# Optimization experiments

Measured on AMD Instinct MI355X. Metric: run time of the kernel, lower is better.

The kernel has to match this reference:

```python
import jax, jax.numpy as jnp
import numpy as np

N, E, H, FN, FE, FO, L = 20000, 50000, 32, 4, 2, 4, 3

def _gelu(v):
    return jax.nn.gelu(v, approximate=False)  # torch nn.GELU default = exact erf

def setup_inputs() -> dict:
    key = jax.random.key(0)
    ks = jax.random.split(key, 24)
    def w(k, shape, fan_in):
        return jax.random.normal(k, shape, dtype=jnp.float32) / np.sqrt(fan_in)
    inp = {
        "x": jax.random.normal(ks[0], (N, FN), dtype=jnp.float32),
        "pred_mask": (jax.random.uniform(ks[1], (N, FN)) < 0.5).astype(jnp.float32),
        "edge_index": jax.random.randint(ks[2], (2, E), 0, N, dtype=jnp.int64),
        "edge_attr": jax.random.normal(ks[3], (E, FE), dtype=jnp.float32),
        # input encoder
        "W_in": w(ks[4], (FN, H), FN), "b_in": jnp.zeros((H,), jnp.float32),
        # mask embedding MLP
        "mW1": w(ks[5], (FN, H), FN), "mb1": jnp.zeros((H,), jnp.float32),
        "mW2": w(ks[6], (H, H), H),   "mb2": jnp.zeros((H,), jnp.float32),
        # per-layer stacked params (leading dim L)
        "eW1": w(ks[7], (L, FE, H), FE),    "eb1": jnp.zeros((L, H), jnp.float32),
        "eW2": w(ks[8], (L, H, H * H), H),  "eb2": jnp.zeros((L, H * H), jnp.float32),
        "W_root": w(ks[9], (L, H, H), H),   "conv_b": jnp.zeros((L, H), jnp.float32),
        "gamma": jnp.ones((L, H), jnp.float32), "beta": jnp.zeros((L, H), jnp.float32),
        # output decoder
        "dW1": w(ks[10], (H, H), H),  "db1": jnp.zeros((H,), jnp.float32),
        "dW2": w(ks[11], (H, FO), H), "db2": jnp.zeros((FO,), jnp.float32),
    }
    return inp

def reference(x, pred_mask, edge_index, edge_attr,
              W_in, b_in, mW1, mb1, mW2, mb2,
              eW1, eb1, eW2, eb2, W_root, conv_b, gamma, beta,
              dW1, db1, dW2, db2):
    # input projection + mask embedding
    h = x @ W_in + b_in + (_gelu(pred_mask @ mW1 + mb1) @ mW2 + mb2)
    # undirect graph (random edge list is directed -> torch path duplicates)
    src = jnp.concatenate([edge_index[0], edge_index[1]])  # [2E]
    dst = jnp.concatenate([edge_index[1], edge_index[0]])
    ea = jnp.concatenate([edge_attr, edge_attr], axis=0)    # [2E, FE]

    def layer(h, p):
        w1, b1, w2, b2, wr, cb, g, b = p
        # edge-conditioned weights: [2E, H, H]
        ew = (_gelu(ea @ w1 + b1) @ w2 + b2).reshape(-1, H, H)
        msg = jnp.einsum('eh,eho->eo', h[src], ew)          # gather + per-edge matvec
        agg = jax.ops.segment_sum(msg, dst, num_segments=N) # scatter-add
        hc = agg + h @ wr + cb                               # NNConv root weight + bias
        mu = jnp.mean(hc, axis=-1, keepdims=True)
        var = jnp.var(hc, axis=-1, keepdims=True)
        hn = (hc - mu) * jax.lax.rsqrt(var + 1e-5) * g + b   # LayerNorm
        return h + _gelu(hn), None                           # dropout in eval mode (no-op)

    h, _ = jax.lax.scan(layer, h, (eW1, eb1, eW2, eb2, W_root, conv_b, gamma, beta))
    out = _gelu(h @ dW1 + db1) @ dW2 + db2
    return out
```

## Files before the change

### kernel.cpp

```cpp
#include <hip/hip_runtime.h>
#include <hip/hip_bf16.h>
#include <math.h>

#define NN  20000
#define NE  50000
#define NE2 100000
#define H   32
#define FN  4
#define FE  2
#define FO  4
#define NL  3

#define FRAGS_PER_LAYER (33 * 2)
#define BVALS_PER_LAYER (FRAGS_PER_LAYER * 512)

#define TCHUNKS 196
#define NB_TALL (NL * 32 * TCHUNKS)
#define NB_PREP ((NL * BVALS_PER_LAYER + 255)/256)
#define NB_ZERO (NN * H / 4 / 256)
#define NB_ENC  ((NN + 255)/256)

typedef __attribute__((ext_vector_type(8))) short short8;
typedef __attribute__((ext_vector_type(4))) float f32x4;

__device__ __forceinline__ float gelu_f(float x) {
    return 0.5f * x * (1.0f + erff(x * 0.7071067811865476f));
}
__device__ __forceinline__ short f2bf(float x) {
    __hip_bfloat16 b = __float2bfloat16(x);
    return __builtin_bit_cast(short, b);
}
__device__ __forceinline__ float bf2f(short s) {
    __hip_bfloat16 b = __builtin_bit_cast(__hip_bfloat16, s);
    return __bfloat162float(b);
}

__global__ __launch_bounds__(256) void prologue(
    const float* __restrict__ x, const float* __restrict__ pm,
    const float* __restrict__ W_in, const float* __restrict__ b_in,
    const float* __restrict__ mW1, const float* __restrict__ mb1,
    const float* __restrict__ mW2, const float* __restrict__ mb2,
    const float* __restrict__ eW1, const float* __restrict__ eb1,
    const float* __restrict__ eW2, const float* __restrict__ eb2,
    const float* __restrict__ ea,
    float* __restrict__ h, float* __restrict__ agg,
    short* __restrict__ Bhi, short* __restrict__ Blo,
    float* __restrict__ tfull)
{
    int bid = blockIdx.x;
    int tid = threadIdx.x;

    if (bid < NB_TALL) {
        int l     = bid / (32 * TCHUNKS);
        int rem   = bid - l * 32 * TCHUNKS;
        int k     = rem / TCHUNKS;
        int chunk = rem - k * TCHUNKS;
        int er    = chunk * 256 + tid;
        float w0 = eW1[l*FE*H + k];
        float w1 = eW1[l*FE*H + H + k];
        float bb = eb1[l*H + k];
        if (er < NE) {
            float tv = gelu_f(ea[er*2] * w0 + ea[er*2+1] * w1 + bb);
            tfull[(l*32 + k) * NE + er] = tv;
        }
        return;
    }
    bid -= NB_TALL;

    if (bid < NB_PREP) {
        int idx = bid * 256 + tid;
        if (idx >= NL * BVALS_PER_LAYER) return;
        int layer = idx / BVALS_PER_LAYER;
        int rem   = idx - layer * BVALS_PER_LAYER;
        int f      = rem >> 9;
        int within = rem & 511;
        int step = f >> 1, nt = f & 1;
        int l = within >> 3, j = within & 7;
        int p = ((l >> 4) << 3) + j;
        int n = nt * 16 + (l & 15);
        float v;
        if (step < 32) v = eW2[layer * 32768 + step * 1024 + p * 32 + n];
        else           v = eb2[layer * 1024 + p * 32 + n];
        short hi = f2bf(v);
        short lo = f2bf(v - bf2f(hi));
        Bhi[idx] = hi;
        Blo[idx] = lo;
        return;
    }
    bid -= NB_PREP;

    if (bid < NB_ZERO) {
        int i = bid * 256 + tid;
        ((float4*)agg)[i] = make_float4(0.f, 0.f, 0.f, 0.f);
        return;
    }
    bid -= NB_ZERO;

    __shared__ float sWin[FN*H], sW1[FN*H], sW2[H*H];
    __shared__ float sbin[H], sb1[H], sb2[H];
    for (int i = tid; i < FN*H; i += 256) { sWin[i] = W_in[i]; sW1[i] = mW1[i]; }
    for (int i = tid; i < H*H; i += 256) sW2[i] = mW2[i];
    if (tid < H) { sbin[tid] = b_in[tid]; sb1[tid] = mb1[tid]; sb2[tid] = mb2[tid]; }
    __syncthreads();
    int n = bid * 256 + tid;
    if (n >= NN) return;
    float xv[FN], pv[FN];
#pragma unroll
    for (int i = 0; i < FN; ++i) { xv[i] = x[n*FN+i]; pv[i] = pm[n*FN+i]; }
    float m[H];
#pragma unroll
    for (int j = 0; j < H; ++j) {
        float a = sb1[j];
#pragma unroll
        for (int i = 0; i < FN; ++i) a += pv[i] * sW1[i*H+j];
        m[j] = gelu_f(a);
    }
#pragma unroll
    for (int j = 0; j < H; ++j) {
        float a = sbin[j] + sb2[j];
#pragma unroll
        for (int i = 0; i < FN; ++i) a += xv[i] * sWin[i*H+j];
        float s = 0.f;
#pragma unroll
        for (int k = 0; k < H; ++k) s += m[k] * sW2[k*H+j];
        h[n*H+j] = a + s;
    }
}

__global__ __launch_bounds__(256) void edge_pass(
    const float* __restrict__ h,
    const int* __restrict__ ei,
    const float* __restrict__ tfull_l,
    const short* __restrict__ Bhi,
    const short* __restrict__ Blo,
    float* __restrict__ agg)
{
    __shared__ float t_lds[32][256];
    __shared__ int src_lds[256], dst_lds[256];

    int tid = threadIdx.x;
    int bid = blockIdx.x;
    bool half2 = bid >= TCHUNKS;
    int er_base = (half2 ? bid - TCHUNKS : bid) * 256;

    {
        int er = er_base + tid;
        int erc = er < NE ? er : NE - 1;
        int s, d;
        if (half2) { s = ei[NE + erc]; d = ei[erc]; }
        else       { s = ei[erc];      d = ei[NE + erc]; }
        bool v = er < NE;
        src_lds[tid] = v ? s : 0;
        dst_lds[tid] = v ? d : 0;
    }
    {
        int c  = tid & 63;
        int kq = tid >> 6;
        int col = er_base + c * 4;
        if (col > NE - 4) col = NE - 4;
#pragma unroll
        for (int q = 0; q < 8; ++q) {
            int k = q * 4 + kq;
            float4 tv = *(const float4*)(tfull_l + k * NE + col);
            *(float4*)&t_lds[k][c * 4] = tv;
        }
    }
    __syncthreads();

    int wv = tid >> 6, lane = tid & 63;
    int lg = lane >> 4, lm = lane & 15;
    int jbase = wv * 64;

    float hs[4][8];
#pragma unroll
    for (int m = 0; m < 4; ++m) {
        int s = src_lds[jbase + m*16 + lm];
        const float4* hp = (const float4*)(h + s*H + lg*8);
        float4 u0 = hp[0], u1 = hp[1];
        hs[m][0]=u0.x; hs[m][1]=u0.y; hs[m][2]=u0.z; hs[m][3]=u0.w;
        hs[m][4]=u1.x; hs[m][5]=u1.y; hs[m][6]=u1.z; hs[m][7]=u1.w;
    }

    f32x4 acc[4][2];
#pragma unroll
    for (int m = 0; m < 4; ++m) {
        acc[m][0] = (f32x4){0.f,0.f,0.f,0.f};
        acc[m][1] = (f32x4){0.f,0.f,0.f,0.f};
    }

    const short8* Bh = (const short8*)Bhi;
    const short8* Bl = (const short8*)Blo;
    short8 cb0h = Bh[lane], cb1h = Bh[64 + lane];
    short8 cb0l = Bl[lane], cb1l = Bl[64 + lane];
    short8 nb0h = cb0h, nb1h = cb1h, nb0l = cb0l, nb1l = cb1l;

#pragma unroll 1
    for (int step = 0; step < 33; ++step) {
        if (step < 32) {
            int fo = (step + 1) * 128 + lane;
            nb0h = Bh[fo]; nb1h = Bh[fo + 64];
            nb0l = Bl[fo]; nb1l = Bl[fo + 64];
        }
#pragma unroll
        for (int m = 0; m < 4; ++m) {
            float tv = (step < 32) ? t_lds[step][jbase + m*16 + lm] : 1.0f;
            short8 a;
#pragma unroll
            for (int j = 0; j < 8; ++j) a[j] = f2bf(tv * hs[m][j]);
            acc[m][0] = __builtin_amdgcn_mfma_f32_16x16x32_bf16(a, cb0h, acc[m][0], 0, 0, 0);
            acc[m][0] = __builtin_amdgcn_mfma_f32_16x16x32_bf16(a, cb0l, acc[m][0], 0, 0, 0);
            acc[m][1] = __builtin_amdgcn_mfma_f32_16x16x32_bf16(a, cb1h, acc[m][1], 0, 0, 0);
            acc[m][1] = __builtin_amdgcn_mfma_f32_16x16x32_bf16(a, cb1l, acc[m][1], 0, 0, 0);
        }
        cb0h = nb0h; cb1h = nb1h; cb0l = nb0l; cb1l = nb1l;
    }

#pragma unroll
    for (int m = 0; m < 4; ++m) {
#pragma unroll
        for (int r = 0; r < 4; ++r) {
            int erow = jbase + m*16 + lg*4 + r;
            if (er_base + erow < NE) {
                int d = dst_lds[erow];
                atomicAdd(agg + d*H + lm,      acc[m][0][r]);
                atomicAdd(agg + d*H + 16 + lm, acc[m][1][r]);
            }
        }
    }
}

__global__ __launch_bounds__(256) void node_update(
    float* __restrict__ h, float* __restrict__ agg,
    const float* __restrict__ wr, const float* __restrict__ cb,
    const float* __restrict__ gamma, const float* __restrict__ beta,
    const float* __restrict__ dW1, const float* __restrict__ db1,
    const float* __restrict__ dW2, const float* __restrict__ db2,
    float* __restrict__ out, int last)
{
    __shared__ float swr[H*H], sW1d[H*H], sW2d[H*FO];
    __shared__ float scb[H], sg[H], sb[H], sb1d[H], sb2d[FO];
    int tid = threadIdx.x;
    for (int i = tid; i < H*H; i += 256) { swr[i] = wr[i]; sW1d[i] = dW1[i]; }
    for (int i = tid; i < H*FO; i += 256) sW2d[i] = dW2[i];
    if (tid < H) { scb[tid] = cb[tid]; sg[tid] = gamma[tid]; sb[tid] = beta[tid]; sb1d[tid] = db1[tid]; }
    if (tid < FO) sb2d[tid] = db2[tid];
    __syncthreads();
    int n = blockIdx.x * 256 + tid;
    if (n >= NN) return;

    float hv[H], hc[H];
#pragma unroll
    for (int q = 0; q < 8; ++q) {
        float4 v = ((const float4*)(h + n*H))[q];
        hv[q*4+0]=v.x; hv[q*4+1]=v.y; hv[q*4+2]=v.z; hv[q*4+3]=v.w;
        float4 g = ((const float4*)(agg + n*H))[q];
        hc[q*4+0]=g.x; hc[q*4+1]=g.y; hc[q*4+2]=g.z; hc[q*4+3]=g.w;
    }
#pragma unroll
    for (int o = 0; o < H; ++o) hc[o] += scb[o];
#pragma unroll
    for (int k = 0; k < H; ++k) {
        float hk = hv[k];
#pragma unroll
        for (int o = 0; o < H; ++o) hc[o] += hk * swr[k*H+o];
    }
    float mu = 0.f;
#pragma unroll
    for (int o = 0; o < H; ++o) mu += hc[o];
    mu *= (1.0f/H);
    float var = 0.f;
#pragma unroll
    for (int o = 0; o < H; ++o) { float d = hc[o]-mu; var += d*d; }
    var *= (1.0f/H);
    float rs = rsqrtf(var + 1e-5f);
#pragma unroll
    for (int o = 0; o < H; ++o) {
        float hn = (hc[o]-mu)*rs*sg[o] + sb[o];
        hv[o] += gelu_f(hn);
    }

    if (!last) {
#pragma unroll
        for (int q = 0; q < 8; ++q) {
            ((float4*)(h + n*H))[q]   = make_float4(hv[q*4+0], hv[q*4+1], hv[q*4+2], hv[q*4+3]);
            ((float4*)(agg + n*H))[q] = make_float4(0.f, 0.f, 0.f, 0.f);
        }
    } else {
        float g[H];
#pragma unroll
        for (int j = 0; j < H; ++j) {
            float a = sb1d[j];
#pragma unroll
            for (int k = 0; k < H; ++k) a += hv[k] * sW1d[k*H+j];
            g[j] = gelu_f(a);
        }
#pragma unroll
        for (int o = 0; o < FO; ++o) {
            float a = sb2d[o];
#pragma unroll
            for (int k = 0; k < H; ++k) a += g[k] * sW2d[k*FO+o];
            out[n*FO+o] = a;
        }
    }
}

extern "C" void kernel_launch(void* const* d_in, const int* in_sizes, int n_in,
                              void* d_out, int out_size, void* d_ws, size_t ws_size,
                              hipStream_t stream)
{
    const float* x    = (const float*)d_in[0];
    const float* pm   = (const float*)d_in[1];
    const int*   ei   = (const int*)d_in[2];
    const float* ea   = (const float*)d_in[3];
    const float* W_in = (const float*)d_in[4];
    const float* b_in = (const float*)d_in[5];
    const float* mW1  = (const float*)d_in[6];
    const float* mb1  = (const float*)d_in[7];
    const float* mW2  = (const float*)d_in[8];
    const float* mb2  = (const float*)d_in[9];
    const float* eW1  = (const float*)d_in[10];
    const float* eb1  = (const float*)d_in[11];
    const float* eW2  = (const float*)d_in[12];
    const float* eb2  = (const float*)d_in[13];
    const float* Wr   = (const float*)d_in[14];
    const float* cb   = (const float*)d_in[15];
    const float* gm   = (const float*)d_in[16];
    const float* bt   = (const float*)d_in[17];
    const float* dW1  = (const float*)d_in[18];
    const float* db1  = (const float*)d_in[19];
    const float* dW2  = (const float*)d_in[20];
    const float* db2  = (const float*)d_in[21];
    float* out = (float*)d_out;

    float* h     = (float*)d_ws;
    float* agg   = h + NN*H;
    float* tfull = agg + NN*H;
    short* Bhi   = (short*)(tfull + NL*32*NE);
    short* Blo   = Bhi + NL * BVALS_PER_LAYER;

    prologue<<<NB_TALL + NB_PREP + NB_ZERO + NB_ENC, 256, 0, stream>>>(
        x, pm, W_in, b_in, mW1, mb1, mW2, mb2, eW1, eb1, eW2, eb2, ea,
        h, agg, Bhi, Blo, tfull);

    for (int l = 0; l < NL; ++l) {
        edge_pass<<<2*TCHUNKS, 256, 0, stream>>>(
            h, ei, tfull + l*32*NE,
            Bhi + l*BVALS_PER_LAYER, Blo + l*BVALS_PER_LAYER, agg);
        node_update<<<(NN + 255)/256, 256, 0, stream>>>(
            h, agg, Wr + l*H*H, cb + l*H, gm + l*H, bt + l*H,
            dW1, db1, dW2, db2, out, l == NL-1);
    }
}
```

Baseline: 181.1 us.

## Fuse all stages into one persistent cooperative kernel with grid syncs

Replaces the prologue plus per-layer edge and node-update launches with a single cooperative kernel on a fixed 256-block grid. Stages are separated by grid-wide barriers, and each stage uses grid-stride loops. Edge tiles shrink to 128 edges and are looped over by the persistent blocks. The aim is to remove per-launch overhead and inter-kernel gaps, at the cost of fixed low occupancy and grid barrier latency. The old multi-kernel path remains as a fallback if the cooperative launch fails.

```diff
diff --git a/kernel.cpp b/kernel.cpp
--- a/kernel.cpp
+++ b/kernel.cpp
@@ -1,6 +1,9 @@
 #include <hip/hip_runtime.h>
+#include <hip/hip_cooperative_groups.h>
 #include <hip/hip_bf16.h>
 #include <math.h>
+
+namespace cg = cooperative_groups;
 
 #define NN  20000
 #define NE  50000
@@ -20,6 +23,11 @@
 #define NB_ZERO (NN * H / 4 / 256)
 #define NB_ENC  ((NN + 255)/256)
 
+#define CGRID 256
+#define EBC   128
+#define TPDC  ((NE + EBC - 1) / EBC)
+#define NTILES (2 * TPDC)
+
 typedef __attribute__((ext_vector_type(8))) short short8;
 typedef __attribute__((ext_vector_type(4))) float f32x4;
 
@@ -33,6 +41,286 @@
 __device__ __forceinline__ float bf2f(short s) {
     __hip_bfloat16 b = __builtin_bit_cast(__hip_bfloat16, s);
     return __bfloat162float(b);
+}
+
+struct Params {
+    const float *x, *pm;
+    const int   *ei;
+    const float *ea;
+    const float *W_in, *b_in, *mW1, *mb1, *mW2, *mb2;
+    const float *eW1, *eb1, *eW2, *eb2;
+    const float *Wr, *cb, *gm, *bt;
+    const float *dW1, *db1, *dW2, *db2;
+    float *out, *h, *agg, *tfull;
+    short *Bhi, *Blo;
+};
+
+__global__ __launch_bounds__(256) void fused_all(Params P)
+{
+    cg::grid_group grid = cg::this_grid();
+    __shared__ __align__(16) unsigned char smem[17536];
+
+    const int tid = threadIdx.x;
+    const int bid = blockIdx.x;
+    const int gid = bid * 256 + tid;
+    const int gstride = CGRID * 256;
+
+    {
+        float* sWin = (float*)smem;
+        float* sW1  = sWin + FN*H;
+        float* sW2  = sW1 + FN*H;
+        float* sbin = sW2 + H*H;
+        float* sb1  = sbin + H;
+        float* sb2  = sb1 + H;
+        for (int i = tid; i < FN*H; i += 256) { sWin[i] = P.W_in[i]; sW1[i] = P.mW1[i]; }
+        for (int i = tid; i < H*H; i += 256) sW2[i] = P.mW2[i];
+        if (tid < H) { sbin[tid] = P.b_in[tid]; sb1[tid] = P.mb1[tid]; sb2[tid] = P.mb2[tid]; }
+        __syncthreads();
+
+        for (int n = gid; n < NN; n += gstride) {
+            float xv[FN], pv[FN];
+#pragma unroll
+            for (int i = 0; i < FN; ++i) { xv[i] = P.x[n*FN+i]; pv[i] = P.pm[n*FN+i]; }
+            float m[H];
+#pragma unroll
+            for (int j = 0; j < H; ++j) {
+                float a = sb1[j];
+#pragma unroll
+                for (int i = 0; i < FN; ++i) a += pv[i] * sW1[i*H+j];
+                m[j] = gelu_f(a);
+            }
+#pragma unroll
+            for (int j = 0; j < H; ++j) {
+                float a = sbin[j] + sb2[j];
+#pragma unroll
+                for (int i = 0; i < FN; ++i) a += xv[i] * sWin[i*H+j];
+                float s = 0.f;
+#pragma unroll
+                for (int k = 0; k < H; ++k) s += m[k] * sW2[k*H+j];
+                P.h[n*H+j] = a + s;
+            }
+        }
+
+        const int U = NL * 32 * (NE / 4);
+        for (int idx = gid; idx < U; idx += gstride) {
+            int lk = idx / (NE / 4);
+            int e4 = idx - lk * (NE / 4);
+            int er = e4 * 4;
+            int l = lk >> 5, k = lk & 31;
+            float w0 = P.eW1[l*FE*H + k];
+            float w1 = P.eW1[l*FE*H + H + k];
+            float bb = P.eb1[l*H + k];
+            float4 q0 = *(const float4*)(P.ea + (size_t)er*2);
+            float4 q1 = *(const float4*)(P.ea + (size_t)er*2 + 4);
+            float4 tv;
+            tv.x = gelu_f(q0.x * w0 + q0.y * w1 + bb);
+            tv.y = gelu_f(q0.z * w0 + q0.w * w1 + bb);
+            tv.z = gelu_f(q1.x * w0 + q1.y * w1 + bb);
+            tv.w = gelu_f(q1.z * w0 + q1.w * w1 + bb);
+            *(float4*)(P.tfull + (size_t)lk * NE + er) = tv;
+        }
+
+        for (int idx = gid; idx < NL * BVALS_PER_LAYER; idx += gstride) {
+            int layer = idx / BVALS_PER_LAYER;
+            int rem   = idx - layer * BVALS_PER_LAYER;
+            int f      = rem >> 9;
+            int within = rem & 511;
+            int step = f >> 1, nt = f & 1;
+            int l = within >> 3, j = within & 7;
+            int p = ((l >> 4) << 3) + j;
+            int n = nt * 16 + (l & 15);
+            float v;
+            if (step < 32) v = P.eW2[layer * 32768 + step * 1024 + p * 32 + n];
+            else           v = P.eb2[layer * 1024 + p * 32 + n];
+            short hi = f2bf(v);
+            short lo = f2bf(v - bf2f(hi));
+            P.Bhi[idx] = hi;
+            P.Blo[idx] = lo;
+        }
+
+        float4 z = make_float4(0.f, 0.f, 0.f, 0.f);
+        for (int i = gid; i < NN * H / 4; i += gstride)
+            ((float4*)P.agg)[i] = z;
+    }
+    grid.sync();
+
+    for (int l = 0; l < NL; ++l) {
+        const float* tfull_l = P.tfull + (size_t)l * 32 * NE;
+        const short8* Bh = (const short8*)(P.Bhi + l * BVALS_PER_LAYER);
+        const short8* Bl = (const short8*)(P.Blo + l * BVALS_PER_LAYER);
+
+        {
+            float (*t_lds)[EBC] = (float(*)[EBC])smem;
+            int* src_lds = (int*)(smem + 32 * EBC * 4);
+            int* dst_lds = src_lds + EBC;
+
+            const int wv = tid >> 6, lane = tid & 63;
+            const int lg = lane >> 4, lm = lane & 15;
+            const int jbase = wv * 32;
+
+            for (int tile = bid; tile < NTILES; tile += CGRID) {
+                __syncthreads();
+                bool half2 = tile >= TPDC;
+                int er_base = (half2 ? tile - TPDC : tile) * EBC;
+
+                if (tid < EBC) {
+                    int er = er_base + tid;
+                    int erc = er < NE ? er : NE - 1;
+                    int s, d;
+                    if (half2) { s = P.ei[NE + erc]; d = P.ei[erc]; }
+                    else       { s = P.ei[erc];      d = P.ei[NE + erc]; }
+                    bool v = er < NE;
+                    src_lds[tid] = v ? s : 0;
+                    dst_lds[tid] = v ? d : 0;
+                }
+                {
+                    int kq = tid >> 5;
+                    int c  = tid & 31;
+                    int col = er_base + c * 4;
+                    if (col > NE - 4) col = NE - 4;
+#pragma unroll
+                    for (int q = 0; q < 4; ++q) {
+                        int k = q * 8 + kq;
+                        *(float4*)&t_lds[k][c * 4] = *(const float4*)(tfull_l + (size_t)k * NE + col);
+                    }
+                }
+                __syncthreads();
+
+                float hs[2][8];
+#pragma unroll
+                for (int m = 0; m < 2; ++m) {
+                    int s = src_lds[jbase + m*16 + lm];
+                    const float4* hp = (const float4*)(P.h + (size_t)s*H + lg*8);
+                    float4 u0 = hp[0], u1 = hp[1];
+                    hs[m][0]=u0.x; hs[m][1]=u0.y; hs[m][2]=u0.z; hs[m][3]=u0.w;
+                    hs[m][4]=u1.x; hs[m][5]=u1.y; hs[m][6]=u1.z; hs[m][7]=u1.w;
+                }
+
+                f32x4 acc[2][2];
+#pragma unroll
+                for (int m = 0; m < 2; ++m) {
+                    acc[m][0] = (f32x4){0.f,0.f,0.f,0.f};
+                    acc[m][1] = (f32x4){0.f,0.f,0.f,0.f};
+                }
+
+                short8 cb0h = Bh[lane], cb1h = Bh[64 + lane];
+                short8 cb0l = Bl[lane], cb1l = Bl[64 + lane];
+                short8 nb0h = cb0h, nb1h = cb1h, nb0l = cb0l, nb1l = cb1l;
+
+#pragma unroll 1
+                for (int step = 0; step < 33; ++step) {
+                    if (step < 32) {
+                        int fo = (step + 1) * 128 + lane;
+                        nb0h = Bh[fo]; nb1h = Bh[fo + 64];
+                        nb0l = Bl[fo]; nb1l = Bl[fo + 64];
+                    }
+#pragma unroll
+                    for (int m = 0; m < 2; ++m) {
+                        float tv = (step < 32) ? t_lds[step][jbase + m*16 + lm] : 1.0f;
+                        short8 a;
+#pragma unroll
+                        for (int j = 0; j < 8; ++j) a[j] = f2bf(tv * hs[m][j]);
+                        acc[m][0] = __builtin_amdgcn_mfma_f32_16x16x32_bf16(a, cb0h, acc[m][0], 0, 0, 0);
+                        acc[m][0] = __builtin_amdgcn_mfma_f32_16x16x32_bf16(a, cb0l, acc[m][0], 0, 0, 0);
+                        acc[m][1] = __builtin_amdgcn_mfma_f32_16x16x32_bf16(a, cb1h, acc[m][1], 0, 0, 0);
+                        acc[m][1] = __builtin_amdgcn_mfma_f32_16x16x32_bf16(a, cb1l, acc[m][1], 0, 0, 0);
+                    }
+                    cb0h = nb0h; cb1h = nb1h; cb0l = nb0l; cb1l = nb1l;
+                }
+
+#pragma unroll
+                for (int m = 0; m < 2; ++m) {
+#pragma unroll
+                    for (int r = 0; r < 4; ++r) {
+                        int erow = jbase + m*16 + lg*4 + r;
+                        if (er_base + erow < NE) {
+                            int d = dst_lds[erow];
+                            atomicAdd(P.agg + (size_t)d*H + lm,      acc[m][0][r]);
+                            atomicAdd(P.agg + (size_t)d*H + 16 + lm, acc[m][1][r]);
+                        }
+                    }
+                }
+            }
+        }
+        grid.sync();
+
+        {
+            float* swr  = (float*)smem;
+            float* sW1d = swr + H*H;
+            float* sW2d = sW1d + H*H;
+            float* scb  = sW2d + H*FO;
+            float* sg   = scb + H;
+            float* sb   = sg + H;
+            float* sb1d = sb + H;
+            float* sb2d = sb1d + H;
+            const int last = (l == NL - 1);
+
+            for (int i = tid; i < H*H; i += 256) { swr[i] = P.Wr[l*H*H + i]; sW1d[i] = P.dW1[i]; }
+            for (int i = tid; i < H*FO; i += 256) sW2d[i] = P.dW2[i];
+            if (tid < H) { scb[tid] = P.cb[l*H + tid]; sg[tid] = P.gm[l*H + tid];
+                           sb[tid] = P.bt[l*H + tid];  sb1d[tid] = P.db1[tid]; }
+            if (tid < FO) sb2d[tid] = P.db2[tid];
+            __syncthreads();
+
+            for (int n = gid; n < NN; n += gstride) {
+                float hv[H], hc[H];
+#pragma unroll
+                for (int q = 0; q < 8; ++q) {
+                    float4 v = ((const float4*)(P.h + (size_t)n*H))[q];
+                    hv[q*4+0]=v.x; hv[q*4+1]=v.y; hv[q*4+2]=v.z; hv[q*4+3]=v.w;
+                    float4 g = ((const float4*)(P.agg + (size_t)n*H))[q];
+                    hc[q*4+0]=g.x; hc[q*4+1]=g.y; hc[q*4+2]=g.z; hc[q*4+3]=g.w;
+                }
+#pragma unroll
+                for (int o = 0; o < H; ++o) hc[o] += scb[o];
+#pragma unroll
+                for (int k = 0; k < H; ++k) {
+                    float hk = hv[k];
+#pragma unroll
+                    for (int o = 0; o < H; ++o) hc[o] += hk * swr[k*H+o];
+                }
+                float mu = 0.f;
+#pragma unroll
+                for (int o = 0; o < H; ++o) mu += hc[o];
+                mu *= (1.0f/H);
+                float var = 0.f;
+#pragma unroll
+                for (int o = 0; o < H; ++o) { float d = hc[o]-mu; var += d*d; }
+                var *= (1.0f/H);
+                float rs = rsqrtf(var + 1e-5f);
+#pragma unroll
+                for (int o = 0; o < H; ++o) {
+                    float hn = (hc[o]-mu)*rs*sg[o] + sb[o];
+                    hv[o] += gelu_f(hn);
+                }
+
+                if (!last) {
+#pragma unroll
+                    for (int q = 0; q < 8; ++q) {
+                        ((float4*)(P.h + (size_t)n*H))[q]   = make_float4(hv[q*4+0], hv[q*4+1], hv[q*4+2], hv[q*4+3]);
+                        ((float4*)(P.agg + (size_t)n*H))[q] = make_float4(0.f, 0.f, 0.f, 0.f);
+                    }
+                } else {
+                    float g[H];
+#pragma unroll
+                    for (int j = 0; j < H; ++j) {
+                        float a = sb1d[j];
+#pragma unroll
+                        for (int k = 0; k < H; ++k) a += hv[k] * sW1d[k*H+j];
+                        g[j] = gelu_f(a);
+                    }
+#pragma unroll
+                    for (int o = 0; o < FO; ++o) {
+                        float a = sb2d[o];
+#pragma unroll
+                        for (int k = 0; k < H; ++k) a += g[k] * sW2d[k*FO+o];
+                        P.out[n*FO+o] = a;
+                    }
+                }
+            }
+        }
+        if (l < NL - 1) grid.sync();
+    }
 }
 
 __global__ __launch_bounds__(256) void prologue(
@@ -308,46 +596,53 @@
                               void* d_out, int out_size, void* d_ws, size_t ws_size,
                               hipStream_t stream)
 {
-    const float* x    = (const float*)d_in[0];
-    const float* pm   = (const float*)d_in[1];
-    const int*   ei   = (const int*)d_in[2];
-    const float* ea   = (const float*)d_in[3];
-    const float* W_in = (const float*)d_in[4];
-    const float* b_in = (const float*)d_in[5];
-    const float* mW1  = (const float*)d_in[6];
-    const float* mb1  = (const float*)d_in[7];
-    const float* mW2  = (const float*)d_in[8];
-    const float* mb2  = (const float*)d_in[9];
-    const float* eW1  = (const float*)d_in[10];
-    const float* eb1  = (const float*)d_in[11];
-    const float* eW2  = (const float*)d_in[12];
-    const float* eb2  = (const float*)d_in[13];
-    const float* Wr   = (const float*)d_in[14];
-    const float* cb   = (const float*)d_in[15];
-    const float* gm   = (const float*)d_in[16];
-    const float* bt   = (const float*)d_in[17];
-    const float* dW1  = (const float*)d_in[18];
-    const float* db1  = (const float*)d_in[19];
-    const float* dW2  = (const float*)d_in[20];
-    const float* db2  = (const float*)d_in[21];
-    float* out = (float*)d_out;
-
-    float* h     = (float*)d_ws;
-    float* agg   = h + NN*H;
-    float* tfull = agg + NN*H;
-    short* Bhi   = (short*)(tfull + NL*32*NE);
-    short* Blo   = Bhi + NL * BVALS_PER_LAYER;
-
-    prologue<<<NB_TALL + NB_PREP + NB_ZERO + NB_ENC, 256, 0, stream>>>(
-        x, pm, W_in, b_in, mW1, mb1, mW2, mb2, eW1, eb1, eW2, eb2, ea,
-        h, agg, Bhi, Blo, tfull);
-
-    for (int l = 0; l < NL; ++l) {
-        edge_pass<<<2*TCHUNKS, 256, 0, stream>>>(
-            h, ei, tfull + l*32*NE,
-            Bhi + l*BVALS_PER_LAYER, Blo + l*BVALS_PER_LAYER, agg);
-        node_update<<<(NN + 255)/256, 256, 0, stream>>>(
-            h, agg, Wr + l*H*H, cb + l*H, gm + l*H, bt + l*H,
-            dW1, db1, dW2, db2, out, l == NL-1);
-    }
-}
+    Params P;
+    P.x    = (const float*)d_in[0];
+    P.pm   = (const float*)d_in[1];
+    P.ei   = (const int*)d_in[2];
+    P.ea   = (const float*)d_in[3];
+    P.W_in = (const float*)d_in[4];
+    P.b_in = (const float*)d_in[5];
+    P.mW1  = (const float*)d_in[6];
+    P.mb1  = (const float*)d_in[7];
+    P.mW2  = (const float*)d_in[8];
+    P.mb2  = (const float*)d_in[9];
+    P.eW1  = (const float*)d_in[10];
+    P.eb1  = (const float*)d_in[11];
+    P.eW2  = (const float*)d_in[12];
+    P.eb2  = (const float*)d_in[13];
+    P.Wr   = (const float*)d_in[14];
+    P.cb   = (const float*)d_in[15];
+    P.gm   = (const float*)d_in[16];
+    P.bt   = (const float*)d_in[17];
+    P.dW1  = (const float*)d_in[18];
+    P.db1  = (const float*)d_in[19];
+    P.dW2  = (const float*)d_in[20];
+    P.db2  = (const float*)d_in[21];
+    P.out  = (float*)d_out;
+
+    P.h     = (float*)d_ws;
+    P.agg   = P.h + NN*H;
+    P.tfull = P.agg + NN*H;
+    P.Bhi   = (short*)(P.tfull + NL*32*NE);
+    P.Blo   = P.Bhi + NL * BVALS_PER_LAYER;
+
+    void* args[] = { &P };
+    hipError_t err = hipLaunchCooperativeKernel((const void*)fused_all,
+                                                dim3(CGRID), dim3(256),
+                                                args, 0, stream);
+    if (err != hipSuccess) {
+        prologue<<<NB_TALL + NB_PREP + NB_ZERO + NB_ENC, 256, 0, stream>>>(
+            P.x, P.pm, P.W_in, P.b_in, P.mW1, P.mb1, P.mW2, P.mb2,
+            P.eW1, P.eb1, P.eW2, P.eb2, P.ea,
+            P.h, P.agg, P.Bhi, P.Blo, P.tfull);
+        for (int l = 0; l < NL; ++l) {
+            edge_pass<<<2*TCHUNKS, 256, 0, stream>>>(
+                P.h, P.ei, P.tfull + (size_t)l*32*NE,
+                P.Bhi + l*BVALS_PER_LAYER, P.Blo + l*BVALS_PER_LAYER, P.agg);
+            node_update<<<(NN + 255)/256, 256, 0, stream>>>(
+                P.h, P.agg, P.Wr + l*H*H, P.cb + l*H, P.gm + l*H, P.bt + l*H,
+                P.dW1, P.db1, P.dW2, P.db2, P.out, l == NL-1);
+        }
+    }
+}
```

New measurement: 479.9 us. 165% more time.

## Fuse edge MLP hidden computation into edge pass and drop bf16 hi/lo split

Applied to the files above, without the earlier changes.

Computes the edge-MLP first layer (gelu of edge_attr projection) directly inside edge_pass into LDS, eliminating the large precomputed tfull buffer and its prologue blocks. Removes the low-order bf16 correction term for the edge weight matrix, halving MFMA count and fragment loads per step, and prefetches fragments two steps ahead. The trade-off is reduced numerical accuracy of the edge-conditioned weights and recomputing gelu per edge in every layer.

```diff
diff --git a/kernel.cpp b/kernel.cpp
--- a/kernel.cpp
+++ b/kernel.cpp
@@ -14,12 +14,13 @@
 #define FRAGS_PER_LAYER (33 * 2)
 #define BVALS_PER_LAYER (FRAGS_PER_LAYER * 512)
 
-#define TCHUNKS 196
-#define NB_TALL (NL * 32 * TCHUNKS)
 #define NB_PREP ((NL * BVALS_PER_LAYER + 255)/256)
 #define NB_ZERO (NN * H / 4 / 256)
 #define NB_ENC  ((NN + 255)/256)
 
+#define TCHUNKS 196
+#define EB      256
+
 typedef __attribute__((ext_vector_type(8))) short short8;
 typedef __attribute__((ext_vector_type(4))) float f32x4;
 
@@ -29,10 +30,6 @@
 __device__ __forceinline__ short f2bf(float x) {
     __hip_bfloat16 b = __float2bfloat16(x);
     return __builtin_bit_cast(short, b);
-}
-__device__ __forceinline__ float bf2f(short s) {
-    __hip_bfloat16 b = __builtin_bit_cast(__hip_bfloat16, s);
-    return __bfloat162float(b);
 }
 
 __global__ __launch_bounds__(256) void prologue(
@@ -40,32 +37,12 @@
     const float* __restrict__ W_in, const float* __restrict__ b_in,
     const float* __restrict__ mW1, const float* __restrict__ mb1,
     const float* __restrict__ mW2, const float* __restrict__ mb2,
-    const float* __restrict__ eW1, const float* __restrict__ eb1,
     const float* __restrict__ eW2, const float* __restrict__ eb2,
-    const float* __restrict__ ea,
     float* __restrict__ h, float* __restrict__ agg,
-    short* __restrict__ Bhi, short* __restrict__ Blo,
-    float* __restrict__ tfull)
+    short* __restrict__ Bhi)
 {
     int bid = blockIdx.x;
     int tid = threadIdx.x;
-
-    if (bid < NB_TALL) {
-        int l     = bid / (32 * TCHUNKS);
-        int rem   = bid - l * 32 * TCHUNKS;
-        int k     = rem / TCHUNKS;
-        int chunk = rem - k * TCHUNKS;
-        int er    = chunk * 256 + tid;
-        float w0 = eW1[l*FE*H + k];
-        float w1 = eW1[l*FE*H + H + k];
-        float bb = eb1[l*H + k];
-        if (er < NE) {
-            float tv = gelu_f(ea[er*2] * w0 + ea[er*2+1] * w1 + bb);
-            tfull[(l*32 + k) * NE + er] = tv;
-        }
-        return;
-    }
-    bid -= NB_TALL;
 
     if (bid < NB_PREP) {
         int idx = bid * 256 + tid;
@@ -81,10 +58,7 @@
         float v;
         if (step < 32) v = eW2[layer * 32768 + step * 1024 + p * 32 + n];
         else           v = eb2[layer * 1024 + p * 32 + n];
-        short hi = f2bf(v);
-        short lo = f2bf(v - bf2f(hi));
-        Bhi[idx] = hi;
-        Blo[idx] = lo;
+        Bhi[idx] = f2bf(v);
         return;
     }
     bid -= NB_PREP;
@@ -130,19 +104,26 @@
 __global__ __launch_bounds__(256) void edge_pass(
     const float* __restrict__ h,
     const int* __restrict__ ei,
-    const float* __restrict__ tfull_l,
+    const float* __restrict__ ea,
+    const float* __restrict__ w1,
+    const float* __restrict__ b1,
     const short* __restrict__ Bhi,
-    const short* __restrict__ Blo,
     float* __restrict__ agg)
 {
-    __shared__ float t_lds[32][256];
-    __shared__ int src_lds[256], dst_lds[256];
+    __shared__ float t_lds[32][EB];
+    __shared__ int src_lds[EB], dst_lds[EB];
+    __shared__ float sw[3*H];
 
     int tid = threadIdx.x;
     int bid = blockIdx.x;
     bool half2 = bid >= TCHUNKS;
-    int er_base = (half2 ? bid - TCHUNKS : bid) * 256;
-
+    int er_base = (half2 ? bid - TCHUNKS : bid) * EB;
+
+    if (tid < H) {
+        sw[tid]       = w1[tid];
+        sw[H + tid]   = w1[H + tid];
+        sw[2*H + tid] = b1[tid];
+    }
     {
         int er = er_base + tid;
         int erc = er < NE ? er : NE - 1;
@@ -153,16 +134,15 @@
         src_lds[tid] = v ? s : 0;
         dst_lds[tid] = v ? d : 0;
     }
+    __syncthreads();
+
     {
-        int c  = tid & 63;
-        int kq = tid >> 6;
-        int col = er_base + c * 4;
-        if (col > NE - 4) col = NE - 4;
-#pragma unroll
-        for (int q = 0; q < 8; ++q) {
-            int k = q * 4 + kq;
-            float4 tv = *(const float4*)(tfull_l + k * NE + col);
-            *(float4*)&t_lds[k][c * 4] = tv;
+        int er = er_base + tid;
+        int erc = er < NE ? er : NE - 1;
+        float2 av = *(const float2*)(ea + (size_t)erc * 2);
+#pragma unroll 8
+        for (int k = 0; k < 32; ++k) {
+            t_lds[k][tid] = gelu_f(av.x * sw[k] + av.y * sw[H + k] + sw[2*H + k]);
         }
     }
     __syncthreads();
@@ -175,7 +155,7 @@
 #pragma unroll
     for (int m = 0; m < 4; ++m) {
         int s = src_lds[jbase + m*16 + lm];
-        const float4* hp = (const float4*)(h + s*H + lg*8);
+        const float4* hp = (const float4*)(h + (size_t)s*H + lg*8);
         float4 u0 = hp[0], u1 = hp[1];
         hs[m][0]=u0.x; hs[m][1]=u0.y; hs[m][2]=u0.z; hs[m][3]=u0.w;
         hs[m][4]=u1.x; hs[m][5]=u1.y; hs[m][6]=u1.z; hs[m][7]=u1.w;
@@ -188,18 +168,16 @@
         acc[m][1] = (f32x4){0.f,0.f,0.f,0.f};
     }
 
-    const short8* Bh = (const short8*)Bhi;
-    const short8* Bl = (const short8*)Blo;
-    short8 cb0h = Bh[lane], cb1h = Bh[64 + lane];
-    short8 cb0l = Bl[lane], cb1l = Bl[64 + lane];
-    short8 nb0h = cb0h, nb1h = cb1h, nb0l = cb0l, nb1l = cb1l;
+    const short8* F = (const short8*)Bhi;
+    short8 A0 = F[lane],        A1 = F[64 + lane];
+    short8 B0 = F[128 + lane],  B1 = F[192 + lane];
+    short8 C0, C1;
 
 #pragma unroll 1
     for (int step = 0; step < 33; ++step) {
-        if (step < 32) {
-            int fo = (step + 1) * 128 + lane;
-            nb0h = Bh[fo]; nb1h = Bh[fo + 64];
-            nb0l = Bl[fo]; nb1l = Bl[fo + 64];
+        if (step + 2 <= 32) {
+            int fo = (step + 2) * 128 + lane;
+            C0 = F[fo]; C1 = F[fo + 64];
         }
 #pragma unroll
         for (int m = 0; m < 4; ++m) {
@@ -207,12 +185,10 @@
             short8 a;
 #pragma unroll
             for (int j = 0; j < 8; ++j) a[j] = f2bf(tv * hs[m][j]);
-            acc[m][0] = __builtin_amdgcn_mfma_f32_16x16x32_bf16(a, cb0h, acc[m][0], 0, 0, 0);
-            acc[m][0] = __builtin_amdgcn_mfma_f32_16x16x32_bf16(a, cb0l, acc[m][0], 0, 0, 0);
-            acc[m][1] = __builtin_amdgcn_mfma_f32_16x16x32_bf16(a, cb1h, acc[m][1], 0, 0, 0);
-            acc[m][1] = __builtin_amdgcn_mfma_f32_16x16x32_bf16(a, cb1l, acc[m][1], 0, 0, 0);
-        }
-        cb0h = nb0h; cb1h = nb1h; cb0l = nb0l; cb1l = nb1l;
+            acc[m][0] = __builtin_amdgcn_mfma_f32_16x16x32_bf16(a, A0, acc[m][0], 0, 0, 0);
+            acc[m][1] = __builtin_amdgcn_mfma_f32_16x16x32_bf16(a, A1, acc[m][1], 0, 0, 0);
+        }
+        A0 = B0; A1 = B1; B0 = C0; B1 = C1;
     }
 
 #pragma unroll
@@ -222,8 +198,8 @@
             int erow = jbase + m*16 + lg*4 + r;
             if (er_base + erow < NE) {
                 int d = dst_lds[erow];
-                atomicAdd(agg + d*H + lm,      acc[m][0][r]);
-                atomicAdd(agg + d*H + 16 + lm, acc[m][1][r]);
+                atomicAdd(agg + (size_t)d*H + lm,      acc[m][0][r]);
+                atomicAdd(agg + (size_t)d*H + 16 + lm, acc[m][1][r]);
             }
         }
     }
@@ -332,20 +308,17 @@
     const float* db2  = (const float*)d_in[21];
     float* out = (float*)d_out;
 
-    float* h     = (float*)d_ws;
-    float* agg   = h + NN*H;
-    float* tfull = agg + NN*H;
-    short* Bhi   = (short*)(tfull + NL*32*NE);
-    short* Blo   = Bhi + NL * BVALS_PER_LAYER;
-
-    prologue<<<NB_TALL + NB_PREP + NB_ZERO + NB_ENC, 256, 0, stream>>>(
-        x, pm, W_in, b_in, mW1, mb1, mW2, mb2, eW1, eb1, eW2, eb2, ea,
-        h, agg, Bhi, Blo, tfull);
+    float* h   = (float*)d_ws;
+    float* agg = h + NN*H;
+    short* Bhi = (short*)(agg + NN*H);
+
+    prologue<<<NB_PREP + NB_ZERO + NB_ENC, 256, 0, stream>>>(
+        x, pm, W_in, b_in, mW1, mb1, mW2, mb2, eW2, eb2, h, agg, Bhi);
 
     for (int l = 0; l < NL; ++l) {
         edge_pass<<<2*TCHUNKS, 256, 0, stream>>>(
-            h, ei, tfull + l*32*NE,
-            Bhi + l*BVALS_PER_LAYER, Blo + l*BVALS_PER_LAYER, agg);
+            h, ei, ea, eW1 + l*FE*H, eb1 + l*H,
+            Bhi + l*BVALS_PER_LAYER, agg);
         node_update<<<(NN + 255)/256, 256, 0, stream>>>(
             h, agg, Wr + l*H*H, cb + l*H, gm + l*H, bt + l*H,
             dW1, db1, dW2, db2, out, l == NL-1);
```

Measured after the change: 155.2 us. 1.17x faster.
